# Optimization experiments

Measured on AMD Instinct MI355X. Metric: run time of the kernel, lower is better.

The kernel has to match this reference:

```python
import jax, jax.numpy as jnp
import numpy as np

S, D, H, DK, DV = 3072, 512, 8, 64, 64
EPS = 1e-6


def entmax15(X):
    """1.5-entmax along the last axis (full-sort algorithm, k=None)."""
    X = X - jnp.max(X, axis=-1, keepdims=True)
    X = X / 2
    Xsrt = -jnp.sort(-X, axis=-1)  # descending sort
    d = X.shape[-1]
    rho = jnp.arange(1, d + 1, dtype=X.dtype)
    mean = jnp.cumsum(Xsrt, axis=-1) / rho
    mean_sq = jnp.cumsum(Xsrt * Xsrt, axis=-1) / rho
    ss = rho * (mean_sq - mean * mean)
    delta = jnp.clip((1.0 - ss) / rho, 0.0, None)
    tau = mean - jnp.sqrt(delta)
    support = jnp.sum(tau <= Xsrt, axis=-1, keepdims=True)  # int
    tau_star = jnp.take_along_axis(tau, support - 1, axis=-1)
    return jnp.square(jnp.clip(X - tau_star, 0.0, None))


def layer_norm(x, gamma, beta):
    mu = jnp.mean(x, axis=-1, keepdims=True)
    var = jnp.mean(jnp.square(x - mu), axis=-1, keepdims=True)
    return (x - mu) / jnp.sqrt(var + EPS) * gamma + beta


def setup_inputs() -> dict:
    key = jax.random.key(0)
    ks = jax.random.split(key, 10)
    s = 0.02
    return {
        "x": jax.random.normal(ks[0], (S, D), dtype=jnp.float32),
        "Wq": jax.random.normal(ks[1], (D, H * DK), dtype=jnp.float32) * s,
        "bq": jnp.zeros((H * DK,), dtype=jnp.float32),
        "Wk": jax.random.normal(ks[2], (D, H * DK), dtype=jnp.float32) * s,
        "bk": jnp.zeros((H * DK,), dtype=jnp.float32),
        "Wv": jax.random.normal(ks[3], (D, H * DV), dtype=jnp.float32) * s,
        "bv": jnp.zeros((H * DV,), dtype=jnp.float32),
        "Wo": jax.random.normal(ks[4], (H * DV, D), dtype=jnp.float32) * s,
        "bo": jnp.zeros((D,), dtype=jnp.float32),
        "gamma": jnp.ones((D,), dtype=jnp.float32),
        "beta": jnp.zeros((D,), dtype=jnp.float32),
    }


def reference(x, Wq, bq, Wk, bk, Wv, bv, Wo, bo, gamma, beta):
    xb = x[None]  # [1, S, D] (module does unsqueeze(0))
    residual = xb
    # QKV projections -> [1, H, S, dk/dv]
    q = (xb @ Wq + bq).reshape(1, S, H, DK).transpose(0, 2, 1, 3)
    k = (xb @ Wk + bk).reshape(1, S, H, DK).transpose(0, 2, 1, 3)
    v = (xb @ Wv + bv).reshape(1, S, H, DV).transpose(0, 2, 1, 3)
    temp = DK ** 0.5
    logits = jnp.einsum("bhqd,bhkd->bhqk", q / temp, k)  # [1,H,S,S]
    attn = entmax15(logits)
    out = jnp.einsum("bhqk,bhkd->bhqd", attn, v)  # [1,H,S,dv]
    out = out.transpose(0, 2, 1, 3).reshape(1, S, H * DV)
    out = out @ Wo + bo
    out = out + residual
    out = layer_norm(out, gamma, beta)  # post-norm (prenorm=False)
    return (out[0], attn)
```

## Files before the change

kernel.cpp:

```cpp
#include <hip/hip_runtime.h>

#define S 3072
#define D 512
#define H 8

constexpr float LN_EPS = 1e-6f;

typedef __attribute__((ext_vector_type(2))) _Float16 f16x2;
typedef __attribute__((ext_vector_type(8))) _Float16 f16x8;
typedef __attribute__((ext_vector_type(4))) float f32x4;

__device__ __forceinline__ f16x2 cvt_pk(float lo, float hi) {
    return __builtin_bit_cast(f16x2, __builtin_amdgcn_cvt_pkrtz(lo, hi));
}

__global__ void prep_w_kernel(const float* __restrict__ Wq, const float* __restrict__ Wk,
                              const float* __restrict__ Wv, const float* __restrict__ Wo,
                              _Float16* __restrict__ WtAll) {
    const int c  = blockIdx.x * 256 + threadIdx.x;
    const int k0 = blockIdx.y * 64;
    const int mat = blockIdx.z;
    const float* W = (mat == 0) ? Wq : (mat == 1) ? Wk : (mat == 2) ? Wv : Wo;
    _Float16* dst = WtAll + ((size_t)(mat * 512 + c)) * 512 + k0;
#pragma unroll
    for (int kb = 0; kb < 8; ++kb) {
        f16x8 v;
#pragma unroll
        for (int i = 0; i < 8; ++i)
            v[i] = (_Float16)W[(size_t)(k0 + kb * 8 + i) * 512 + c];
        *(f16x8*)(dst + kb * 8) = v;
    }
}

__global__ void prep_x_kernel(const float* __restrict__ x, _Float16* __restrict__ xh) {
    const int i = blockIdx.x * 256 + threadIdx.x;
    const float4* xf = (const float4*)x;
    float4 a = xf[i * 2], b = xf[i * 2 + 1];
    f16x8 v = {(_Float16)a.x, (_Float16)a.y, (_Float16)a.z, (_Float16)a.w,
               (_Float16)b.x, (_Float16)b.y, (_Float16)b.z, (_Float16)b.w};
    *(f16x8*)(xh + (size_t)i * 8) = v;
}

__global__ __launch_bounds__(256) void qkv_mfma_kernel(
        const _Float16* __restrict__ xh, const _Float16* __restrict__ WtAll,
        const float* __restrict__ bq, const float* __restrict__ bk,
        const float* __restrict__ bv,
        _Float16* __restrict__ Qb, _Float16* __restrict__ Kb,
        _Float16* __restrict__ Vt) {
    const int t = threadIdx.x;
    const int w = t >> 6, l = t & 63, lr = l & 15, lk = l >> 4;
    const int r0 = blockIdx.x * 64 + w * 16;
    const int c0 = blockIdx.y * 64;
    const _Float16* Ar = xh + (size_t)(r0 + lr) * 512 + lk * 8;
    const _Float16* Br = WtAll + (size_t)(c0 + lr) * 512 + lk * 8;

    f32x4 acc[4];
#pragma unroll
    for (int j = 0; j < 4; ++j) acc[j] = (f32x4){0.f, 0.f, 0.f, 0.f};
    for (int ks = 0; ks < 16; ++ks) {
        f16x8 a = *(const f16x8*)(Ar + ks * 32);
#pragma unroll
        for (int j = 0; j < 4; ++j) {
            f16x8 b = *(const f16x8*)(Br + (size_t)(j * 16) * 512 + ks * 32);
            acc[j] = __builtin_amdgcn_mfma_f32_16x16x32_f16(a, b, acc[j], 0, 0, 0);
        }
    }
    const int m = c0 >> 9;
    const float* bias = (m == 0) ? bq : (m == 1) ? bk : bv;
#pragma unroll
    for (int j = 0; j < 4; ++j) {
        const int cc = (c0 & 511) + j * 16 + lr;
        const int h = cc >> 6, d = cc & 63;
        const float bb_ = bias[cc];
#pragma unroll
        for (int r = 0; r < 4; ++r) {
            const int row = r0 + lk * 4 + r;
            float val = acc[j][r] + bb_;
            if (m == 0)      Qb[((size_t)h * S + row) * 64 + d] = (_Float16)(val * 0.0625f);
            else if (m == 1) Kb[((size_t)h * S + row) * 64 + d] = (_Float16)val;
            else {
                int bb = row & 31;
                int sp = (row & ~31) | (((bb & 15) << 1) | (bb >> 4));
                Vt[((size_t)h * 64 + d) * S + sp] = (_Float16)val;
            }
        }
    }
}

__global__ __launch_bounds__(512, 4) void fused_attn_kernel(
        const _Float16* __restrict__ Qb, const _Float16* __restrict__ Kb,
        const _Float16* __restrict__ Vt, float* __restrict__ attn,
        _Float16* __restrict__ AOh) {
    __shared__ float sred[2][8][16][3];
    __shared__ __align__(16) f16x2 plds[2][8][16][20];
    __shared__ float pacc[16][64];
    const int bid = blockIdx.x;
    const int h = bid & 7, qt = bid >> 3;
    const int q0 = qt * 16;
    const int t = threadIdx.x;
    const int w = t >> 6, l = t & 63;
    const int lr = l & 15, lk = l >> 4;
    const int kbase = w * 384;

    ((float*)pacc)[t] = 0.f;
    ((float*)pacc)[t + 512] = 0.f;

    const _Float16* Qh = Qb + ((size_t)h * S) * 64;
    const _Float16* Kh = Kb + ((size_t)h * S) * 64;
    const _Float16* Vh = Vt + (size_t)h * 64 * S;

    const f16x8 aq0 = *(const f16x8*)(Qh + (size_t)(q0 + lr) * 64 + lk * 8);
    const f16x8 aq1 = *(const f16x8*)(Qh + (size_t)(q0 + lr) * 64 + 32 + lk * 8);

    const f16x2 one2  = {(_Float16)1.f, (_Float16)1.f};
    const f16x2 zero2 = {(_Float16)0.f, (_Float16)0.f};
    const f16x2 big2  = {(_Float16)16384.f, (_Float16)16384.f};

    f16x2 zw[12][4];
    f16x2 m2[4];
    float s4[4] = {}, q4[4] = {};
#pragma unroll
    for (int r = 0; r < 4; ++r) m2[r] = (f16x2){(_Float16)-60000.f, (_Float16)-60000.f};
#pragma unroll
    for (int jp = 0; jp < 12; ++jp) {
        const _Float16* kp = Kh + (size_t)(kbase + jp * 32 + lr) * 64;
        f16x8 b00 = *(const f16x8*)(kp + lk * 8);
        f16x8 b01 = *(const f16x8*)(kp + 32 + lk * 8);
        f16x8 b10 = *(const f16x8*)(kp + 16 * 64 + lk * 8);
        f16x8 b11 = *(const f16x8*)(kp + 16 * 64 + 32 + lk * 8);
        f32x4 d0 = (f32x4){0.f, 0.f, 0.f, 0.f}, d1 = d0;
        d0 = __builtin_amdgcn_mfma_f32_16x16x32_f16(aq0, b00, d0, 0, 0, 0);
        d0 = __builtin_amdgcn_mfma_f32_16x16x32_f16(aq1, b01, d0, 0, 0, 0);
        d1 = __builtin_amdgcn_mfma_f32_16x16x32_f16(aq0, b10, d1, 0, 0, 0);
        d1 = __builtin_amdgcn_mfma_f32_16x16x32_f16(aq1, b11, d1, 0, 0, 0);
#pragma unroll
        for (int r = 0; r < 4; ++r) {
            f16x2 w2 = cvt_pk(d0[r], d1[r]);
            zw[jp][r] = w2;
            m2[r] = __builtin_elementwise_max(m2[r], w2);
            s4[r] = __builtin_amdgcn_fdot2(w2, one2, s4[r], false);
            q4[r] = __builtin_amdgcn_fdot2(w2, w2, q4[r], false);
        }
    }
    float m4[4];
#pragma unroll
    for (int r = 0; r < 4; ++r) m4[r] = fmaxf((float)m2[r][0], (float)m2[r][1]);
#pragma unroll
    for (int off = 1; off < 16; off <<= 1) {
#pragma unroll
        for (int r = 0; r < 4; ++r) {
            m4[r] = fmaxf(m4[r], __shfl_xor(m4[r], off, 64));
            s4[r] += __shfl_xor(s4[r], off, 64);
            q4[r] += __shfl_xor(q4[r], off, 64);
        }
    }
    if (lr == 0) {
#pragma unroll
        for (int r = 0; r < 4; ++r) {
            sred[0][w][lk * 4 + r][0] = m4[r];
            sred[0][w][lk * 4 + r][1] = s4[r];
            sred[0][w][lk * 4 + r][2] = q4[r];
        }
    }
    __syncthreads();

    const float n = (float)S;
    float Tj;
    {
        float mj = -1e30f, sj = 0.f, qj = 0.f;
#pragma unroll
        for (int ww = 0; ww < 8; ++ww) {
            mj = fmaxf(mj, sred[0][ww][lr][0]);
            sj += sred[0][ww][lr][1];
            qj += sred[0][ww][lr][2];
        }
        float mean = sj * (1.f / n);
        float msq  = qj * (1.f / n);
        float ssv  = n * (msq - mean * mean);
        Tj = mean - sqrtf(fmaxf((1.f - ssv) / n, 0.f));
        Tj = fminf(fmaxf(Tj, mj - 1.0f), mj - 0.01f);
    }
    float T4[4];
#pragma unroll
    for (int r = 0; r < 4; ++r) T4[r] = __shfl(Tj, lk * 4 + r, 64);

    for (int it = 0; it < 8; ++it) {
        const int buf = (it + 1) & 1;
        f16x2 T2[4];
#pragma unroll
        for (int r = 0; r < 4; ++r) T2[r] = cvt_pk(T4[r], T4[r]);
        float f4[4] = {}, fp4[4] = {}, cn4[4] = {};
#pragma unroll
        for (int jp = 0; jp < 12; ++jp)
#pragma unroll
            for (int r = 0; r < 4; ++r) {
                f16x2 zc = __builtin_elementwise_max(zw[jp][r] - T2[r], zero2);
                f4[r]  = __builtin_amdgcn_fdot2(zc, zc, f4[r], false);
                fp4[r] = __builtin_amdgcn_fdot2(zc, one2, fp4[r], false);
                f16x2 g = __builtin_elementwise_min(zc * big2, one2);
                cn4[r] = __builtin_amdgcn_fdot2(g, one2, cn4[r], false);
            }
#pragma unroll
        for (int off = 1; off < 16; off <<= 1) {
#pragma unroll
            for (int r = 0; r < 4; ++r) {
                f4[r]  += __shfl_xor(f4[r],  off, 64);
                fp4[r] += __shfl_xor(fp4[r], off, 64);
                cn4[r] += __shfl_xor(cn4[r], off, 64);
            }
        }
        if (lr == 0) {
#pragma unroll
            for (int r = 0; r < 4; ++r) {
                sred[buf][w][lk * 4 + r][0] = f4[r];
                sred[buf][w][lk * 4 + r][1] = fp4[r];
                sred[buf][w][lk * 4 + r][2] = cn4[r];
            }
        }
        __syncthreads();
        float fj = 0.f, fpj = 0.f, cnj = 0.f;
#pragma unroll
        for (int ww = 0; ww < 8; ++ww) {
            fj  += sred[buf][ww][lr][0];
            fpj += sred[buf][ww][lr][1];
            cnj += sred[buf][ww][lr][2];
        }
        float ns   = fmaxf(cnj, 1.0f);
        float disc = fmaxf(fpj * fpj - ns * (fj - 1.0f), 0.f);
        float del  = (fpj - sqrtf(disc)) / ns;
#pragma unroll
        for (int r = 0; r < 4; ++r) T4[r] += __shfl(del, lk * 4 + r, 64);
        if (__all(fabsf(del) < 2e-6f)) break;
    }

    f16x2 T2[4];
#pragma unroll
    for (int r = 0; r < 4; ++r) T2[r] = cvt_pk(T4[r], T4[r]);
    float* arow_t = attn + ((size_t)h * S + q0 + lr) * S + kbase + lk * 4;
    const _Float16* vp0 = Vh + (size_t)(0 * 16 + lr) * S + kbase + lk * 8;
    const _Float16* vp1 = Vh + (size_t)(1 * 16 + lr) * S + kbase + lk * 8;
    const _Float16* vp2 = Vh + (size_t)(2 * 16 + lr) * S + kbase + lk * 8;
    const _Float16* vp3 = Vh + (size_t)(3 * 16 + lr) * S + kbase + lk * 8;
    f32x4 acc[4];
#pragma unroll
    for (int j = 0; j < 4; ++j) acc[j] = (f32x4){0.f, 0.f, 0.f, 0.f};
#pragma unroll
    for (int jp = 0; jp < 12; ++jp) {
        const int buf = jp & 1;
        union { f16x2 h2[4]; f16x8 v; } pw;
#pragma unroll
        for (int r = 0; r < 4; ++r) {
            f16x2 zc = __builtin_elementwise_max(zw[jp][r] - T2[r], zero2);
            pw.h2[r] = zc * zc;
        }
        *(f16x8*)&plds[buf][w][lr][lk * 4] = pw.v;
        union { f16x2 h2[4]; f16x8 v; } au;
#pragma unroll
        for (int u = 0; u < 4; ++u) au.h2[u] = plds[buf][w][lk * 4 + u][lr];
        f32x4 lo = {(float)au.v[0], (float)au.v[2], (float)au.v[4], (float)au.v[6]};
        f32x4 hi = {(float)au.v[1], (float)au.v[3], (float)au.v[5], (float)au.v[7]};
        __builtin_nontemporal_store(lo, (f32x4*)(arow_t + jp * 32));
        __builtin_nontemporal_store(hi, (f32x4*)(arow_t + jp * 32 + 16));
        acc[0] = __builtin_amdgcn_mfma_f32_16x16x32_f16(au.v, *(const f16x8*)(vp0 + jp * 32), acc[0], 0, 0, 0);
        acc[1] = __builtin_amdgcn_mfma_f32_16x16x32_f16(au.v, *(const f16x8*)(vp1 + jp * 32), acc[1], 0, 0, 0);
        acc[2] = __builtin_amdgcn_mfma_f32_16x16x32_f16(au.v, *(const f16x8*)(vp2 + jp * 32), acc[2], 0, 0, 0);
        acc[3] = __builtin_amdgcn_mfma_f32_16x16x32_f16(au.v, *(const f16x8*)(vp3 + jp * 32), acc[3], 0, 0, 0);
    }
#pragma unroll
    for (int j = 0; j < 4; ++j)
#pragma unroll
        for (int r = 0; r < 4; ++r)
            atomicAdd(&pacc[lk * 4 + r][j * 16 + lr], acc[j][r]);
    __syncthreads();
    _Float16* AOr = AOh + (size_t)q0 * 512 + h * 64;
#pragma unroll
    for (int u = 0; u < 2; ++u) {
        int idx = t + 512 * u;
        int row = idx >> 6, col = idx & 63;
        AOr[(size_t)row * 512 + col] = (_Float16)pacc[row][col];
    }
}

__global__ __launch_bounds__(512) void outproj_mfma_kernel(
        const _Float16* __restrict__ AOh, const _Float16* __restrict__ WtAll,
        const float* __restrict__ bo, const float* __restrict__ x,
        const float* __restrict__ gamma, const float* __restrict__ beta,
        float* __restrict__ out) {
    __shared__ float red[8][16][2];
    const int s0 = blockIdx.x * 16;
    const int t = threadIdx.x, w = t >> 6, l = t & 63;
    const int lr = l & 15, lk = l >> 4;
    const _Float16* Ar = AOh + (size_t)(s0 + lr) * 512 + lk * 8;
    const _Float16* Br = WtAll + (size_t)(1536 + w * 64 + lr) * 512 + lk * 8;

    f32x4 acc[4];
#pragma unroll
    for (int j = 0; j < 4; ++j) acc[j] = (f32x4){0.f, 0.f, 0.f, 0.f};
    for (int ks = 0; ks < 16; ++ks) {
        f16x8 a = *(const f16x8*)(Ar + ks * 32);
#pragma unroll
        for (int j = 0; j < 4; ++j) {
            f16x8 b = *(const f16x8*)(Br + (size_t)(j * 16) * 512 + ks * 32);
            acc[j] = __builtin_amdgcn_mfma_f32_16x16x32_f16(a, b, acc[j], 0, 0, 0);
        }
    }
    float s_[4] = {}, q_[4] = {};
#pragma unroll
    for (int j = 0; j < 4; ++j) {
        const int col = w * 64 + j * 16 + lr;
        const float b0 = bo[col];
#pragma unroll
        for (int r = 0; r < 4; ++r) {
            float y = acc[j][r] + b0 + x[(size_t)(s0 + lk * 4 + r) * 512 + col];
            acc[j][r] = y;
            s_[r] += y;
            q_[r] = fmaf(y, y, q_[r]);
        }
    }
#pragma unroll
    for (int off = 1; off < 16; off <<= 1) {
#pragma unroll
        for (int r = 0; r < 4; ++r) {
            s_[r] += __shfl_xor(s_[r], off, 64);
            q_[r] += __shfl_xor(q_[r], off, 64);
        }
    }
    if (lr == 0) {
#pragma unroll
        for (int r = 0; r < 4; ++r) {
            red[w][lk * 4 + r][0] = s_[r];
            red[w][lk * 4 + r][1] = q_[r];
        }
    }
    __syncthreads();
#pragma unroll
    for (int r = 0; r < 4; ++r) {
        const int rowi = lk * 4 + r;
        float sj = 0.f, qj = 0.f;
#pragma unroll
        for (int ww = 0; ww < 8; ++ww) { sj += red[ww][rowi][0]; qj += red[ww][rowi][1]; }
        float mu  = sj * (1.0f / 512.0f);
        float var = qj * (1.0f / 512.0f) - mu * mu;
        float inv = rsqrtf(var + LN_EPS);
        const size_t rbase = (size_t)(s0 + rowi) * 512;
#pragma unroll
        for (int j = 0; j < 4; ++j) {
            const int col = w * 64 + j * 16 + lr;
            out[rbase + col] = (acc[j][r] - mu) * inv * gamma[col] + beta[col];
        }
    }
}

extern "C" void kernel_launch(void* const* d_in, const int* in_sizes, int n_in,
                              void* d_out, int out_size, void* d_ws, size_t ws_size,
                              hipStream_t stream) {
    const float* x     = (const float*)d_in[0];
    const float* Wq    = (const float*)d_in[1];
    const float* bq    = (const float*)d_in[2];
    const float* Wk    = (const float*)d_in[3];
    const float* bk    = (const float*)d_in[4];
    const float* Wv    = (const float*)d_in[5];
    const float* bv    = (const float*)d_in[6];
    const float* Wo    = (const float*)d_in[7];
    const float* bo    = (const float*)d_in[8];
    const float* gamma = (const float*)d_in[9];
    const float* beta  = (const float*)d_in[10];

    float* out  = (float*)d_out;
    float* attn = out + (size_t)S * D;

    _Float16* Qb    = (_Float16*)d_ws;
    _Float16* Kb    = Qb + (size_t)H * S * 64;
    _Float16* Vt    = Kb + (size_t)H * S * 64;
    _Float16* xh    = Vt + (size_t)H * S * 64;
    _Float16* WtAll = xh + (size_t)S * 512;
    _Float16* AOh   = WtAll + (size_t)2048 * 512;

    prep_w_kernel<<<dim3(2, 8, 4), 256, 0, stream>>>(Wq, Wk, Wv, Wo, WtAll);
    prep_x_kernel<<<dim3(S * D / 2048), 256, 0, stream>>>(x, xh);
    qkv_mfma_kernel<<<dim3(48, 24), 256, 0, stream>>>(xh, WtAll, bq, bk, bv, Qb, Kb, Vt);
    fused_attn_kernel<<<dim3((S / 16) * H), 512, 0, stream>>>(Qb, Kb, Vt, attn, AOh);
    outproj_mfma_kernel<<<dim3(S / 16), 512, 0, stream>>>(AOh, WtAll, bo, x, gamma, beta, out);
}
```

Measured before the change: 326.6 us.

## Switch entmax threshold solve to Newton iteration and split P·V loop

Measured after the change: 270.6 us, median of 2. 17.1% less time.

```diff
diff --git a/kernel.cpp b/kernel.cpp
--- a/kernel.cpp
+++ b/kernel.cpp
@@ -91,7 +91,8 @@
         const _Float16* __restrict__ Qb, const _Float16* __restrict__ Kb,
         const _Float16* __restrict__ Vt, float* __restrict__ attn,
         _Float16* __restrict__ AOh) {
-    __shared__ float sred[2][8][16][3];
+    __shared__ float sred[2][8][16][2];
+    __shared__ float smax[8][16];
     __shared__ __align__(16) f16x2 plds[2][8][16][20];
     __shared__ float pacc[16][64];
     const int bid = blockIdx.x;
@@ -114,7 +115,6 @@
 
     const f16x2 one2  = {(_Float16)1.f, (_Float16)1.f};
     const f16x2 zero2 = {(_Float16)0.f, (_Float16)0.f};
-    const f16x2 big2  = {(_Float16)16384.f, (_Float16)16384.f};
 
     f16x2 zw[12][4];
     f16x2 m2[4];
@@ -157,9 +157,9 @@
     if (lr == 0) {
 #pragma unroll
         for (int r = 0; r < 4; ++r) {
-            sred[0][w][lk * 4 + r][0] = m4[r];
-            sred[0][w][lk * 4 + r][1] = s4[r];
-            sred[0][w][lk * 4 + r][2] = q4[r];
+            smax[w][lk * 4 + r]        = m4[r];
+            sred[0][w][lk * 4 + r][0]  = s4[r];
+            sred[0][w][lk * 4 + r][1]  = q4[r];
         }
     }
     __syncthreads();
@@ -170,9 +170,9 @@
         float mj = -1e30f, sj = 0.f, qj = 0.f;
 #pragma unroll
         for (int ww = 0; ww < 8; ++ww) {
-            mj = fmaxf(mj, sred[0][ww][lr][0]);
-            sj += sred[0][ww][lr][1];
-            qj += sred[0][ww][lr][2];
+            mj = fmaxf(mj, smax[ww][lr]);
+            sj += sred[0][ww][lr][0];
+            qj += sred[0][ww][lr][1];
         }
         float mean = sj * (1.f / n);
         float msq  = qj * (1.f / n);
@@ -184,12 +184,12 @@
 #pragma unroll
     for (int r = 0; r < 4; ++r) T4[r] = __shfl(Tj, lk * 4 + r, 64);
 
-    for (int it = 0; it < 8; ++it) {
+    for (int it = 0; it < 6; ++it) {
         const int buf = (it + 1) & 1;
         f16x2 T2[4];
 #pragma unroll
         for (int r = 0; r < 4; ++r) T2[r] = cvt_pk(T4[r], T4[r]);
-        float f4[4] = {}, fp4[4] = {}, cn4[4] = {};
+        float f4[4] = {}, fp4[4] = {};
 #pragma unroll
         for (int jp = 0; jp < 12; ++jp)
 #pragma unroll
@@ -197,8 +197,6 @@
                 f16x2 zc = __builtin_elementwise_max(zw[jp][r] - T2[r], zero2);
                 f4[r]  = __builtin_amdgcn_fdot2(zc, zc, f4[r], false);
                 fp4[r] = __builtin_amdgcn_fdot2(zc, one2, fp4[r], false);
-                f16x2 g = __builtin_elementwise_min(zc * big2, one2);
-                cn4[r] = __builtin_amdgcn_fdot2(g, one2, cn4[r], false);
             }
 #pragma unroll
         for (int off = 1; off < 16; off <<= 1) {
@@ -206,7 +204,6 @@
             for (int r = 0; r < 4; ++r) {
                 f4[r]  += __shfl_xor(f4[r],  off, 64);
                 fp4[r] += __shfl_xor(fp4[r], off, 64);
-                cn4[r] += __shfl_xor(cn4[r], off, 64);
             }
         }
         if (lr == 0) {
@@ -214,36 +211,27 @@
             for (int r = 0; r < 4; ++r) {
                 sred[buf][w][lk * 4 + r][0] = f4[r];
                 sred[buf][w][lk * 4 + r][1] = fp4[r];
-                sred[buf][w][lk * 4 + r][2] = cn4[r];
             }
         }
         __syncthreads();
-        float fj = 0.f, fpj = 0.f, cnj = 0.f;
+        float fj = 0.f, fpj = 0.f;
 #pragma unroll
         for (int ww = 0; ww < 8; ++ww) {
             fj  += sred[buf][ww][lr][0];
             fpj += sred[buf][ww][lr][1];
-            cnj += sred[buf][ww][lr][2];
-        }
-        float ns   = fmaxf(cnj, 1.0f);
-        float disc = fmaxf(fpj * fpj - ns * (fj - 1.0f), 0.f);
-        float del  = (fpj - sqrtf(disc)) / ns;
-#pragma unroll
-        for (int r = 0; r < 4; ++r) T4[r] += __shfl(del, lk * 4 + r, 64);
-        if (__all(fabsf(del) < 2e-6f)) break;
+        }
+        float del = (fj - 1.0f) / (2.0f * fpj + 1e-20f);
+        Tj += del;
+#pragma unroll
+        for (int r = 0; r < 4; ++r) T4[r] = __shfl(Tj, lk * 4 + r, 64);
+        if (__all(fabsf(del) < 1e-6f)) break;
     }
 
     f16x2 T2[4];
 #pragma unroll
     for (int r = 0; r < 4; ++r) T2[r] = cvt_pk(T4[r], T4[r]);
     float* arow_t = attn + ((size_t)h * S + q0 + lr) * S + kbase + lk * 4;
-    const _Float16* vp0 = Vh + (size_t)(0 * 16 + lr) * S + kbase + lk * 8;
-    const _Float16* vp1 = Vh + (size_t)(1 * 16 + lr) * S + kbase + lk * 8;
-    const _Float16* vp2 = Vh + (size_t)(2 * 16 + lr) * S + kbase + lk * 8;
-    const _Float16* vp3 = Vh + (size_t)(3 * 16 + lr) * S + kbase + lk * 8;
-    f32x4 acc[4];
-#pragma unroll
-    for (int j = 0; j < 4; ++j) acc[j] = (f32x4){0.f, 0.f, 0.f, 0.f};
+    f16x8 azw[12];
 #pragma unroll
     for (int jp = 0; jp < 12; ++jp) {
         const int buf = jp & 1;
@@ -257,20 +245,26 @@
         union { f16x2 h2[4]; f16x8 v; } au;
 #pragma unroll
         for (int u = 0; u < 4; ++u) au.h2[u] = plds[buf][w][lk * 4 + u][lr];
+        azw[jp] = au.v;
         f32x4 lo = {(float)au.v[0], (float)au.v[2], (float)au.v[4], (float)au.v[6]};
         f32x4 hi = {(float)au.v[1], (float)au.v[3], (float)au.v[5], (float)au.v[7]};
         __builtin_nontemporal_store(lo, (f32x4*)(arow_t + jp * 32));
         __builtin_nontemporal_store(hi, (f32x4*)(arow_t + jp * 32 + 16));
-        acc[0] = __builtin_amdgcn_mfma_f32_16x16x32_f16(au.v, *(const f16x8*)(vp0 + jp * 32), acc[0], 0, 0, 0);
-        acc[1] = __builtin_amdgcn_mfma_f32_16x16x32_f16(au.v, *(const f16x8*)(vp1 + jp * 32), acc[1], 0, 0, 0);
-        acc[2] = __builtin_amdgcn_mfma_f32_16x16x32_f16(au.v, *(const f16x8*)(vp2 + jp * 32), acc[2], 0, 0, 0);
-        acc[3] = __builtin_amdgcn_mfma_f32_16x16x32_f16(au.v, *(const f16x8*)(vp3 + jp * 32), acc[3], 0, 0, 0);
-    }
-#pragma unroll
-    for (int j = 0; j < 4; ++j)
+    }
+
+#pragma unroll
+    for (int j = 0; j < 4; ++j) {
+        const _Float16* vpj = Vh + (size_t)(j * 16 + lr) * S + kbase + lk * 8;
+        f32x4 a4 = (f32x4){0.f, 0.f, 0.f, 0.f};
+#pragma unroll
+        for (int jp = 0; jp < 12; ++jp) {
+            f16x8 b = *(const f16x8*)(vpj + jp * 32);
+            a4 = __builtin_amdgcn_mfma_f32_16x16x32_f16(azw[jp], b, a4, 0, 0, 0);
+        }
 #pragma unroll
         for (int r = 0; r < 4; ++r)
-            atomicAdd(&pacc[lk * 4 + r][j * 16 + lr], acc[j][r]);
+            atomicAdd(&pacc[lk * 4 + r][j * 16 + lr], a4[r]);
+    }
     __syncthreads();
     _Float16* AOr = AOh + (size_t)q0 * 512 + h * 64;
 #pragma unroll
```
